# Kernel optimization log

Hardware: AMD Instinct MI355X
Metric: run time of the kernel (lower is better)

Reference implementation:

```python
import math
import jax, jax.numpy as jnp
import numpy as np

B, T, C = 2, 2048, 1024
N_HEAD = 16
HEAD_DIM = C // N_HEAD


def setup_inputs() -> dict:
    key = jax.random.key(0)
    k1, k2, k3 = jax.random.split(key, 3)
    std = 0.02
    return {
        "x": jax.random.normal(k1, (B, T, C), dtype=jnp.float32),
        "W_qkv": jax.random.normal(k2, (3 * C, C), dtype=jnp.float32) * std,
        "b_qkv": jnp.zeros((3 * C,), dtype=jnp.float32),
        "W_proj": jax.random.normal(k3, (C, C), dtype=jnp.float32) * std,
        "b_proj": jnp.zeros((C,), dtype=jnp.float32),
    }


def reference(x, W_qkv, b_qkv, W_proj, b_proj):
    Bs, Ts, Cs = x.shape
    # qkv projection, split as [3][n_head][head_dim] along last dim (matches torch view order)
    qkv = (x @ W_qkv.T + b_qkv).reshape(Bs, Ts, 3, N_HEAD, HEAD_DIM)
    qkv = qkv.transpose(0, 3, 2, 1, 4)  # (B, H, 3, T, hd)
    q, k, v = qkv[:, :, 0], qkv[:, :, 1], qkv[:, :, 2]  # each (B, H, T, hd)
    scale = 1.0 / math.sqrt(HEAD_DIM)
    att = jnp.einsum('bhtd,bhsd->bhts', q, k) * scale  # (B, H, T, T)
    causal = jnp.tril(jnp.ones((Ts, Ts), dtype=bool))
    att = jnp.where(causal, att, -jnp.inf)
    att = jax.nn.softmax(att, axis=-1)
    y = jnp.einsum('bhts,bhsd->bhtd', att, v)  # (B, H, T, hd)
    y = y.transpose(0, 2, 1, 3).reshape(Bs, Ts, Cs)
    return y @ W_proj.T + b_proj
```

## Files before the change

### kernel.cpp

```cpp
#include <hip/hip_runtime.h>
#include <cstdint>

#define BDIM  2
#define TSEQ  2048
#define CDIM  1024
#define NHEAD 16
#define HDIM  64
#define C3    3072

typedef __attribute__((ext_vector_type(8))) short short8_t;
typedef __attribute__((ext_vector_type(4))) short short4_t;
typedef __attribute__((ext_vector_type(4))) float f32x4;

static __device__ __forceinline__ unsigned short f2bf(float f) {
  union { float f; unsigned u; } v; v.f = f;
  unsigned r = v.u + 0x7FFFu + ((v.u >> 16) & 1u);
  return (unsigned short)(r >> 16);
}
static __device__ __forceinline__ unsigned cvtpk_bf16(float lo, float hi) {
  unsigned r;
  asm("v_cvt_pk_bf16_f32 %0, %1, %2" : "=v"(r) : "v"(lo), "v"(hi));
  return r;
}
static __device__ __forceinline__ void g2lds16(const unsigned short* g,
                                               unsigned short* l) {
  __builtin_amdgcn_global_load_lds(
      (const __attribute__((address_space(1))) void*)g,
      (__attribute__((address_space(3))) void*)l, 16, 0, 0);
}

__device__ __forceinline__ int kk_idx(int row, int chunk) {
  return row * 64 + (((chunk ^ (row & 7)) & 7) << 3);
}
__device__ __forceinline__ int vv_idx(int d, int chunk) {
  return d * 64 + (((chunk ^ (d & 7) ^ ((d >> 3) & 7)) & 7) << 3);
}

__global__ __launch_bounds__(256) void f32_to_bf16_3(
    const float* __restrict__ x, const float* __restrict__ wq,
    const float* __restrict__ wp, unsigned short* __restrict__ outb,
    int n1, int n2, int n3)
{
  const int i = blockIdx.x * 256 + threadIdx.x;
  const float* src; unsigned short* dst; int j;
  if (i < n1)            { src = x;  dst = outb;                        j = i; }
  else if (i < n1 + n2)  { src = wq; dst = outb + (size_t)n1 * 4;       j = i - n1; }
  else if (i < n1+n2+n3) { src = wp; dst = outb + (size_t)(n1+n2) * 4;  j = i - n1 - n2; }
  else return;
  const float4 v = ((const float4*)src)[j];
  const unsigned lo = (unsigned)f2bf(v.x) | ((unsigned)f2bf(v.y) << 16);
  const unsigned hi = (unsigned)f2bf(v.z) | ((unsigned)f2bf(v.w) << 16);
  ((uint2*)dst)[j] = make_uint2(lo, hi);
}

template <int FJ, bool OUT_BF16, int MWPE>
__global__ __launch_bounds__(256, MWPE) void gemm_bt_mfma(
    const unsigned short* __restrict__ A, const unsigned short* __restrict__ B,
    const float* __restrict__ bias, void* __restrict__ Cv,
    int M, int N, int K)
{
  __shared__ unsigned short As[128 * 64];
  __shared__ unsigned short Bs[FJ * 32 * 64];

  const int tid  = threadIdx.x;
  const int lane = tid & 63;
  const int wv   = tid >> 6;
  const int wr   = wv >> 1, wc = wv & 1;
  const int l15  = lane & 15, g = lane >> 4;
  const int bn = blockIdx.x, bm = blockIdx.y;

  const int srow = tid >> 3;
  const int chg  = (tid & 7) ^ (srow & 7);
  const unsigned short* Ab = A + (size_t)(bm * 128 + srow) * K + chg * 8;
  const unsigned short* Bb = B + (size_t)(bn * (FJ * 32) + srow) * K + chg * 8;

  f32x4 acc[4][FJ];
#pragma unroll
  for (int i = 0; i < 4; ++i)
#pragma unroll
    for (int j = 0; j < FJ; ++j) acc[i][j] = (f32x4){0.f, 0.f, 0.f, 0.f};

  for (int k0 = 0; k0 < K; k0 += 64) {
    __syncthreads();
#pragma unroll
    for (int c = 0; c < 4; ++c)
      g2lds16(Ab + (size_t)(c * 32) * K + k0, &As[c * 2048 + wv * 512]);
#pragma unroll
    for (int c = 0; c < FJ; ++c)
      g2lds16(Bb + (size_t)(c * 32) * K + k0, &Bs[c * 2048 + wv * 512]);
    __syncthreads();

#pragma unroll
    for (int kk = 0; kk < 2; ++kk) {
      short8_t af[4], bf[FJ];
#pragma unroll
      for (int i = 0; i < 4; ++i)
        af[i] = *(const short8_t*)&As[kk_idx(wr * 64 + i * 16 + l15, kk * 4 + g)];
#pragma unroll
      for (int j = 0; j < FJ; ++j)
        bf[j] = *(const short8_t*)&Bs[kk_idx(wc * (FJ * 16) + j * 16 + l15, kk * 4 + g)];
#pragma unroll
      for (int i = 0; i < 4; ++i)
#pragma unroll
        for (int j = 0; j < FJ; ++j)
          acc[i][j] = __builtin_amdgcn_mfma_f32_16x16x32_bf16(af[i], bf[j], acc[i][j], 0, 0, 0);
    }
  }

#pragma unroll
  for (int j = 0; j < FJ; ++j) {
    const int col = bn * (FJ * 32) + wc * (FJ * 16) + j * 16 + l15;
    const float bj = bias[col];
#pragma unroll
    for (int i = 0; i < 4; ++i) {
#pragma unroll
      for (int r = 0; r < 4; ++r) {
        const int row = bm * 128 + wr * 64 + i * 16 + g * 4 + r;
        const float v = acc[i][j][r] + bj;
        if (OUT_BF16) ((unsigned short*)Cv)[(size_t)row * N + col] = f2bf(v);
        else          ((float*)Cv)[(size_t)row * N + col] = v;
      }
    }
  }
}

__global__ __launch_bounds__(512, 8) void attn_mfma(
    const unsigned short* __restrict__ qkv, unsigned short* __restrict__ yb)
{
  __shared__ unsigned short SM[21504];
  unsigned short* Ks = SM;
  unsigned short* Vt = SM + 8192;
  unsigned short* Ps = SM + 16384;

  const int tid  = threadIdx.x;
  const int lane = tid & 63;
  const int wv   = tid >> 6;
  const int qs   = wv & 3;
  const int kvh  = wv >> 2;
  const int l15  = lane & 15, g = lane >> 4;

  const int nfl = blockIdx.x;
  const int x   = (nfl >> 3) & 15;
  const int grp = (nfl & 7) | ((nfl >> 7) << 3);
  const int h = grp & 15, b = grp >> 4;

  const unsigned short* kbase = qkv + (size_t)(b * TSEQ) * C3 + CDIM + h * HDIM;
  const unsigned short* vbase = kbase + CDIM;
  unsigned short* Pw = &Ps[wv * 640];

  const float SC2 = 0.18033688011112042f;
  const float THR = 11.5415603f;

  const int skv = tid >> 3, sc = tid & 7;
  const int kwo = kk_idx(skv, sc);
  const int vs = tid >> 4, dh = (tid >> 3) & 1, va = tid & 7;
  int vwo[4];
#pragma unroll
  for (int j = 0; j < 4; ++j)
    vwo[j] = vv_idx(va * 8 + dh * 4 + j, vs >> 2) + ((2 * vs) & 7);

  int tg = 0;

  for (int ph = 0; ph < 2; ++ph) {
    const int qt   = ph ? (31 - x) : x;
    const int wq0  = qt * 64 + qs * 16;
    const int q_hi = wq0 + 15;
    const int qg   = wq0 + l15;

    short8_t qf[2];
#pragma unroll
    for (int kk = 0; kk < 2; ++kk)
      qf[kk] = *(const short8_t*)(qkv +
          (size_t)(b * TSEQ + wq0 + l15) * C3 + h * HDIM + kk * 32 + g * 8);

    f32x4 O[4];
#pragma unroll
    for (int n = 0; n < 4; ++n) O[n] = (f32x4){0.f, 0.f, 0.f, 0.f};
    float Mr = 0.0f, Lr = 0.f;

    const unsigned short* kptr  = kbase + (size_t)skv * C3 + sc * 8;
    const unsigned short* vptr0 = vbase + (size_t)(2 * vs) * C3 + va * 8 + dh * 4;
    const unsigned short* vptr1 = vptr0 + C3;
    short8_t pk  = *(const short8_t*)(kptr);
    short4_t pv0 = *(const short4_t*)(vptr0);
    short4_t pv1 = *(const short4_t*)(vptr1);

    for (int t = 0; t < qt; ++t) {
      const int par = tg & 1;
      unsigned short* Kc = &Ks[par * 4096];
      unsigned short* Vc = &Vt[par * 4096];
      tg++;
      *(short8_t*)&Kc[kwo] = pk;
      {
        const unsigned short* e0 = (const unsigned short*)&pv0;
        const unsigned short* e1 = (const unsigned short*)&pv1;
#pragma unroll
        for (int j = 0; j < 4; ++j)
          *(unsigned*)&Vc[vwo[j]] = (unsigned)e0[j] | ((unsigned)e1[j] << 16);
      }
      __syncthreads();
      kptr  += (size_t)64 * C3;
      vptr0 += (size_t)64 * C3;
      vptr1 += (size_t)64 * C3;
      pk  = *(const short8_t*)(kptr);
      pv0 = *(const short4_t*)(vptr0);
      pv1 = *(const short4_t*)(vptr1);

      f32x4 s[2];
#pragma unroll
      for (int n = 0; n < 2; ++n) s[n] = (f32x4){0.f, 0.f, 0.f, 0.f};
      __builtin_amdgcn_s_setprio(1);
#pragma unroll
      for (int n = 0; n < 2; ++n) {
#pragma unroll
        for (int kk = 0; kk < 2; ++kk) {
          const short8_t kf =
              *(const short8_t*)&Kc[kk_idx(kvh * 32 + n * 16 + l15, kk * 4 + g)];
          s[n] = __builtin_amdgcn_mfma_f32_16x16x32_bf16(kf, qf[kk], s[n], 0, 0, 0);
        }
      }
      __builtin_amdgcn_s_setprio(0);

      float mt = -3.0e38f, rs = 0.f;
#pragma unroll
      for (int n = 0; n < 2; ++n)
#pragma unroll
        for (int r = 0; r < 4; ++r) mt = fmaxf(mt, s[n][r]);
#pragma unroll
      for (int n = 0; n < 2; ++n)
#pragma unroll
        for (int r = 0; r < 4; ++r) {
          const float p = __builtin_amdgcn_exp2f(fmaf(s[n][r], SC2, -Mr));
          s[n][r] = p;
          rs += p;
        }
#pragma unroll
      for (int n = 0; n < 2; ++n) {
        const unsigned u0 = cvtpk_bf16(s[n][0], s[n][1]);
        const unsigned u1 = cvtpk_bf16(s[n][2], s[n][3]);
        *(uint2*)&Pw[l15 * 40 + n * 16 + (g << 2)] = make_uint2(u0, u1);
      }
      mt *= SC2;
      mt = fmaxf(mt, __shfl_xor(mt, 16));
      mt = fmaxf(mt, __shfl_xor(mt, 32));
      if (__any(mt > Mr + THR)) {
        const float nm = fmaxf(Mr, mt);
        const float al = __builtin_amdgcn_exp2f(Mr - nm);
        Lr *= al;
        rs *= al;
        float alq[4];
#pragma unroll
        for (int r = 0; r < 4; ++r) alq[r] = __shfl(al, (g << 2) + r);
#pragma unroll
        for (int n = 0; n < 4; ++n)
#pragma unroll
          for (int r = 0; r < 4; ++r) O[n][r] *= alq[r];
        Mr = nm;
#pragma unroll
        for (int n = 0; n < 2; ++n) {
#pragma unroll
          for (int r = 0; r < 4; ++r) s[n][r] *= al;
          const unsigned u0 = cvtpk_bf16(s[n][0], s[n][1]);
          const unsigned u1 = cvtpk_bf16(s[n][2], s[n][3]);
          *(uint2*)&Pw[l15 * 40 + n * 16 + (g << 2)] = make_uint2(u0, u1);
        }
      }

      const short8_t pf = *(const short8_t*)&Pw[l15 * 40 + g * 8];
      __builtin_amdgcn_s_setprio(1);
#pragma unroll
      for (int n = 0; n < 4; ++n) {
        const short8_t vf = *(const short8_t*)&Vc[vv_idx(n * 16 + l15, kvh * 4 + g)];
        O[n] = __builtin_amdgcn_mfma_f32_16x16x32_bf16(pf, vf, O[n], 0, 0, 0);
      }
      __builtin_amdgcn_s_setprio(0);

      rs += __shfl_xor(rs, 16);
      rs += __shfl_xor(rs, 32);
      Lr += rs;
    }

    {
      const int t = qt;
      const int par = tg & 1;
      unsigned short* Kc = &Ks[par * 4096];
      unsigned short* Vc = &Vt[par * 4096];
      tg++;
      *(short8_t*)&Kc[kwo] = pk;
      {
        const unsigned short* e0 = (const unsigned short*)&pv0;
        const unsigned short* e1 = (const unsigned short*)&pv1;
#pragma unroll
        for (int j = 0; j < 4; ++j)
          *(unsigned*)&Vc[vwo[j]] = (unsigned)e0[j] | ((unsigned)e1[j] << 16);
      }
      __syncthreads();
      const int kvw0 = t * 64 + kvh * 32;
      if (kvw0 <= q_hi) {
        const int nl = (q_hi - kvw0) >> 4;
        const int nlim = (nl > 1) ? 1 : nl;

        f32x4 s[2];
#pragma unroll
        for (int n = 0; n < 2; ++n) s[n] = (f32x4){0.f, 0.f, 0.f, 0.f};
        __builtin_amdgcn_s_setprio(1);
#pragma unroll
        for (int n = 0; n < 2; ++n) {
          if (n <= nlim) {
#pragma unroll
            for (int kk = 0; kk < 2; ++kk) {
              const short8_t kf =
                  *(const short8_t*)&Kc[kk_idx(kvh * 32 + n * 16 + l15, kk * 4 + g)];
              s[n] = __builtin_amdgcn_mfma_f32_16x16x32_bf16(kf, qf[kk], s[n], 0, 0, 0);
            }
          }
        }
        __builtin_amdgcn_s_setprio(0);

        float mt = -3.0e38f;
#pragma unroll
        for (int n = 0; n < 2; ++n) {
          if (n <= nlim) {
            const int kvb = kvw0 + n * 16 + g * 4;
            const bool needmask = (kvw0 + n * 16 + 15 > wq0);
#pragma unroll
            for (int r = 0; r < 4; ++r) {
              float v = s[n][r] * SC2;
              if (needmask && (kvb + r > qg)) v = -3.0e38f;
              s[n][r] = v;
              mt = fmaxf(mt, v);
            }
          }
        }
        float rs = 0.f;
#pragma unroll
        for (int n = 0; n < 2; ++n) {
          if (n <= nlim) {
#pragma unroll
            for (int r = 0; r < 4; ++r) {
              const float p = __builtin_amdgcn_exp2f(s[n][r] - Mr);
              s[n][r] = p;
              rs += p;
            }
          }
        }
#pragma unroll
        for (int n = 0; n < 2; ++n) {
          const unsigned u0 = cvtpk_bf16(s[n][0], s[n][1]);
          const unsigned u1 = cvtpk_bf16(s[n][2], s[n][3]);
          *(uint2*)&Pw[l15 * 40 + n * 16 + (g << 2)] = make_uint2(u0, u1);
        }
        mt = fmaxf(mt, __shfl_xor(mt, 16));
        mt = fmaxf(mt, __shfl_xor(mt, 32));
        if (__any(mt > Mr + THR)) {
          const float nm = fmaxf(Mr, mt);
          const float al = __builtin_amdgcn_exp2f(Mr - nm);
          Lr *= al;
          rs *= al;
          float alq[4];
#pragma unroll
          for (int r = 0; r < 4; ++r) alq[r] = __shfl(al, (g << 2) + r);
#pragma unroll
          for (int n = 0; n < 4; ++n)
#pragma unroll
            for (int r = 0; r < 4; ++r) O[n][r] *= alq[r];
          Mr = nm;
#pragma unroll
          for (int n = 0; n < 2; ++n) {
            if (n <= nlim) {
#pragma unroll
              for (int r = 0; r < 4; ++r) s[n][r] *= al;
            }
            const unsigned u0 = cvtpk_bf16(s[n][0], s[n][1]);
            const unsigned u1 = cvtpk_bf16(s[n][2], s[n][3]);
            *(uint2*)&Pw[l15 * 40 + n * 16 + (g << 2)] = make_uint2(u0, u1);
          }
        }

        const short8_t pf = *(const short8_t*)&Pw[l15 * 40 + g * 8];
        __builtin_amdgcn_s_setprio(1);
#pragma unroll
        for (int n = 0; n < 4; ++n) {
          const short8_t vf = *(const short8_t*)&Vc[vv_idx(n * 16 + l15, kvh * 4 + g)];
          O[n] = __builtin_amdgcn_mfma_f32_16x16x32_bf16(pf, vf, O[n], 0, 0, 0);
        }
        __builtin_amdgcn_s_setprio(0);

        rs += __shfl_xor(rs, 16);
        rs += __shfl_xor(rs, 32);
        Lr += rs;
      }
    }

    __syncthreads();
    {
      float* Cb = (float*)SM;
      const int slot = (qs * 64 + lane) * 18;
      if (kvh == 1) {
#pragma unroll
        for (int n = 0; n < 4; ++n)
#pragma unroll
          for (int r = 0; r < 4; ++r) Cb[slot + n * 4 + r] = O[n][r];
        Cb[slot + 16] = Mr;
        Cb[slot + 17] = Lr;
      }
    }
    __syncthreads();
    if (kvh == 0) {
      const float* Cb = (const float*)SM;
      const int slot = (qs * 64 + lane) * 18;
      const float m2 = Cb[slot + 16], l2 = Cb[slot + 17];
      const float m  = fmaxf(Mr, m2);
      const float a1 = __builtin_amdgcn_exp2f(Mr - m);
      const float a2 = __builtin_amdgcn_exp2f(m2 - m);
      const float inv = 1.0f / (Lr * a1 + l2 * a2);
      const float fa = a1 * inv, fb = a2 * inv;
      float faq[4], fbq[4];
#pragma unroll
      for (int r = 0; r < 4; ++r) {
        faq[r] = __shfl(fa, (g << 2) + r);
        fbq[r] = __shfl(fb, (g << 2) + r);
      }
#pragma unroll
      for (int n = 0; n < 4; ++n)
#pragma unroll
        for (int r = 0; r < 4; ++r) {
          const float o2 = Cb[slot + n * 4 + r];
          const size_t row = (size_t)(b * TSEQ + wq0 + (g << 2) + r);
          yb[row * CDIM + h * HDIM + n * 16 + l15] =
              f2bf(O[n][r] * faq[r] + o2 * fbq[r]);
        }
    }
    __syncthreads();
  }
}

extern "C" void kernel_launch(void* const* d_in, const int* in_sizes, int n_in,
                              void* d_out, int out_size, void* d_ws, size_t ws_size,
                              hipStream_t stream)
{
  const float* x     = (const float*)d_in[0];
  const float* Wqkv  = (const float*)d_in[1];
  const float* bqkv  = (const float*)d_in[2];
  const float* Wproj = (const float*)d_in[3];
  const float* bproj = (const float*)d_in[4];
  float* out = (float*)d_out;

  const int M = BDIM * TSEQ;
  unsigned short* qkv = (unsigned short*)d_ws;
  unsigned short* yb  = qkv + (size_t)M * C3;
  unsigned short* xb  = yb  + (size_t)M * CDIM;
  unsigned short* wqb = xb  + (size_t)M * CDIM;
  unsigned short* wpb = wqb + (size_t)C3 * CDIM;

  const int n1 = M * CDIM / 4, n2 = C3 * CDIM / 4, n3 = CDIM * CDIM / 4;
  f32_to_bf16_3<<<(n1 + n2 + n3 + 255) / 256, 256, 0, stream>>>(
      x, Wqkv, Wproj, xb, n1, n2, n3);

  gemm_bt_mfma<4, true, 3><<<dim3(C3 / 128, M / 128), 256, 0, stream>>>(
      xb, wqb, bqkv, (void*)qkv, M, C3, CDIM);

  attn_mfma<<<dim3(512, 1, 1), 512, 0, stream>>>(qkv, yb);

  gemm_bt_mfma<2, false, 2><<<dim3(CDIM / 64, M / 128), 256, 0, stream>>>(
      yb, wpb, bproj, (void*)out, M, CDIM, CDIM);
}
```

Baseline: 97.27 us.

## Process two KV tiles per barrier with quad-buffered K/V shared memory

The attention loop now stages two 64-row K/V tiles per iteration into four LDS buffers. This halves the number of __syncthreads barriers and doubles the global prefetch depth. In exchange LDS use grows from about 42KB to about 74KB per block, which may limit occupancy. The final diagonal step now handles a 128-row chunk and may load tiles past the causal boundary.

Result: no change. 96.95 us (-0.3%).

```diff
diff --git a/kernel.cpp b/kernel.cpp
--- a/kernel.cpp
+++ b/kernel.cpp
@@ -127,10 +127,10 @@
 __global__ __launch_bounds__(512, 8) void attn_mfma(
     const unsigned short* __restrict__ qkv, unsigned short* __restrict__ yb)
 {
-  __shared__ unsigned short SM[21504];
+  __shared__ unsigned short SM[37888];
   unsigned short* Ks = SM;
-  unsigned short* Vt = SM + 8192;
-  unsigned short* Ps = SM + 16384;
+  unsigned short* Vt = SM + 16384;
+  unsigned short* Ps = SM + 32768;
 
   const int tid  = threadIdx.x;
   const int lane = tid & 63;
@@ -159,13 +159,12 @@
   for (int j = 0; j < 4; ++j)
     vwo[j] = vv_idx(va * 8 + dh * 4 + j, vs >> 2) + ((2 * vs) & 7);
 
-  int tg = 0;
-
   for (int ph = 0; ph < 2; ++ph) {
     const int qt   = ph ? (31 - x) : x;
     const int wq0  = qt * 64 + qs * 16;
     const int q_hi = wq0 + 15;
     const int qg   = wq0 + l15;
+    const int fastc = qt >> 1;
 
     short8_t qf[2];
 #pragma unroll
@@ -180,123 +179,149 @@
 
     const unsigned short* kptr  = kbase + (size_t)skv * C3 + sc * 8;
     const unsigned short* vptr0 = vbase + (size_t)(2 * vs) * C3 + va * 8 + dh * 4;
-    const unsigned short* vptr1 = vptr0 + C3;
-    short8_t pk  = *(const short8_t*)(kptr);
+    short8_t pk0 = *(const short8_t*)(kptr);
+    short8_t pk1 = *(const short8_t*)(kptr + (size_t)64 * C3);
     short4_t pv0 = *(const short4_t*)(vptr0);
-    short4_t pv1 = *(const short4_t*)(vptr1);
-
-    for (int t = 0; t < qt; ++t) {
-      const int par = tg & 1;
-      unsigned short* Kc = &Ks[par * 4096];
-      unsigned short* Vc = &Vt[par * 4096];
-      tg++;
-      *(short8_t*)&Kc[kwo] = pk;
+    short4_t pv1 = *(const short4_t*)(vptr0 + C3);
+    short4_t pv2 = *(const short4_t*)(vptr0 + (size_t)64 * C3);
+    short4_t pv3 = *(const short4_t*)(vptr0 + (size_t)65 * C3);
+
+    for (int c = 0; c < fastc; ++c) {
+      const int p2 = (c & 1) << 1;
       {
+        unsigned short* K0 = &Ks[p2 * 4096];
+        unsigned short* K1 = &Ks[(p2 + 1) * 4096];
+        unsigned short* V0 = &Vt[p2 * 4096];
+        unsigned short* V1 = &Vt[(p2 + 1) * 4096];
+        *(short8_t*)&K0[kwo] = pk0;
+        *(short8_t*)&K1[kwo] = pk1;
         const unsigned short* e0 = (const unsigned short*)&pv0;
         const unsigned short* e1 = (const unsigned short*)&pv1;
-#pragma unroll
-        for (int j = 0; j < 4; ++j)
-          *(unsigned*)&Vc[vwo[j]] = (unsigned)e0[j] | ((unsigned)e1[j] << 16);
+        const unsigned short* e2 = (const unsigned short*)&pv2;
+        const unsigned short* e3 = (const unsigned short*)&pv3;
+#pragma unroll
+        for (int j = 0; j < 4; ++j) {
+          *(unsigned*)&V0[vwo[j]] = (unsigned)e0[j] | ((unsigned)e1[j] << 16);
+          *(unsigned*)&V1[vwo[j]] = (unsigned)e2[j] | ((unsigned)e3[j] << 16);
+        }
       }
       __syncthreads();
-      kptr  += (size_t)64 * C3;
-      vptr0 += (size_t)64 * C3;
-      vptr1 += (size_t)64 * C3;
-      pk  = *(const short8_t*)(kptr);
+      kptr  += (size_t)128 * C3;
+      vptr0 += (size_t)128 * C3;
+      pk0 = *(const short8_t*)(kptr);
+      pk1 = *(const short8_t*)(kptr + (size_t)64 * C3);
       pv0 = *(const short4_t*)(vptr0);
-      pv1 = *(const short4_t*)(vptr1);
-
-      f32x4 s[2];
-#pragma unroll
-      for (int n = 0; n < 2; ++n) s[n] = (f32x4){0.f, 0.f, 0.f, 0.f};
-      __builtin_amdgcn_s_setprio(1);
-#pragma unroll
-      for (int n = 0; n < 2; ++n) {
-#pragma unroll
-        for (int kk = 0; kk < 2; ++kk) {
-          const short8_t kf =
-              *(const short8_t*)&Kc[kk_idx(kvh * 32 + n * 16 + l15, kk * 4 + g)];
-          s[n] = __builtin_amdgcn_mfma_f32_16x16x32_bf16(kf, qf[kk], s[n], 0, 0, 0);
-        }
-      }
-      __builtin_amdgcn_s_setprio(0);
-
-      float mt = -3.0e38f, rs = 0.f;
-#pragma unroll
-      for (int n = 0; n < 2; ++n)
-#pragma unroll
-        for (int r = 0; r < 4; ++r) mt = fmaxf(mt, s[n][r]);
-#pragma unroll
-      for (int n = 0; n < 2; ++n)
-#pragma unroll
-        for (int r = 0; r < 4; ++r) {
-          const float p = __builtin_amdgcn_exp2f(fmaf(s[n][r], SC2, -Mr));
-          s[n][r] = p;
-          rs += p;
-        }
-#pragma unroll
-      for (int n = 0; n < 2; ++n) {
-        const unsigned u0 = cvtpk_bf16(s[n][0], s[n][1]);
-        const unsigned u1 = cvtpk_bf16(s[n][2], s[n][3]);
-        *(uint2*)&Pw[l15 * 40 + n * 16 + (g << 2)] = make_uint2(u0, u1);
-      }
-      mt *= SC2;
-      mt = fmaxf(mt, __shfl_xor(mt, 16));
-      mt = fmaxf(mt, __shfl_xor(mt, 32));
-      if (__any(mt > Mr + THR)) {
-        const float nm = fmaxf(Mr, mt);
-        const float al = __builtin_amdgcn_exp2f(Mr - nm);
-        Lr *= al;
-        rs *= al;
-        float alq[4];
-#pragma unroll
-        for (int r = 0; r < 4; ++r) alq[r] = __shfl(al, (g << 2) + r);
-#pragma unroll
-        for (int n = 0; n < 4; ++n)
-#pragma unroll
-          for (int r = 0; r < 4; ++r) O[n][r] *= alq[r];
-        Mr = nm;
-#pragma unroll
-        for (int n = 0; n < 2; ++n) {
-#pragma unroll
-          for (int r = 0; r < 4; ++r) s[n][r] *= al;
+      pv1 = *(const short4_t*)(vptr0 + C3);
+      pv2 = *(const short4_t*)(vptr0 + (size_t)64 * C3);
+      pv3 = *(const short4_t*)(vptr0 + (size_t)65 * C3);
+
+#pragma unroll
+      for (int sub = 0; sub < 2; ++sub) {
+        const unsigned short* Kc = &Ks[(p2 + sub) * 4096];
+        const unsigned short* Vc = &Vt[(p2 + sub) * 4096];
+
+        f32x4 s[2];
+#pragma unroll
+        for (int n = 0; n < 2; ++n) s[n] = (f32x4){0.f, 0.f, 0.f, 0.f};
+        __builtin_amdgcn_s_setprio(1);
+#pragma unroll
+        for (int n = 0; n < 2; ++n) {
+#pragma unroll
+          for (int kk = 0; kk < 2; ++kk) {
+            const short8_t kf =
+                *(const short8_t*)&Kc[kk_idx(kvh * 32 + n * 16 + l15, kk * 4 + g)];
+            s[n] = __builtin_amdgcn_mfma_f32_16x16x32_bf16(kf, qf[kk], s[n], 0, 0, 0);
+          }
+        }
+        __builtin_amdgcn_s_setprio(0);
+
+        float mt = -3.0e38f, rs = 0.f;
+#pragma unroll
+        for (int n = 0; n < 2; ++n)
+#pragma unroll
+          for (int r = 0; r < 4; ++r) mt = fmaxf(mt, s[n][r]);
+#pragma unroll
+        for (int n = 0; n < 2; ++n)
+#pragma unroll
+          for (int r = 0; r < 4; ++r) {
+            const float p = __builtin_amdgcn_exp2f(fmaf(s[n][r], SC2, -Mr));
+            s[n][r] = p;
+            rs += p;
+          }
+#pragma unroll
+        for (int n = 0; n < 2; ++n) {
           const unsigned u0 = cvtpk_bf16(s[n][0], s[n][1]);
           const unsigned u1 = cvtpk_bf16(s[n][2], s[n][3]);
           *(uint2*)&Pw[l15 * 40 + n * 16 + (g << 2)] = make_uint2(u0, u1);
         }
-      }
-
-      const short8_t pf = *(const short8_t*)&Pw[l15 * 40 + g * 8];
-      __builtin_amdgcn_s_setprio(1);
-#pragma unroll
-      for (int n = 0; n < 4; ++n) {
-        const short8_t vf = *(const short8_t*)&Vc[vv_idx(n * 16 + l15, kvh * 4 + g)];
-        O[n] = __builtin_amdgcn_mfma_f32_16x16x32_bf16(pf, vf, O[n], 0, 0, 0);
-      }
-      __builtin_amdgcn_s_setprio(0);
-
-      rs += __shfl_xor(rs, 16);
-      rs += __shfl_xor(rs, 32);
-      Lr += rs;
+        mt *= SC2;
+        mt = fmaxf(mt, __shfl_xor(mt, 16));
+        mt = fmaxf(mt, __shfl_xor(mt, 32));
+        if (__any(mt > Mr + THR)) {
+          const float nm = fmaxf(Mr, mt);
+          const float al = __builtin_amdgcn_exp2f(Mr - nm);
+          Lr *= al;
+          rs *= al;
+          float alq[4];
+#pragma unroll
+          for (int r = 0; r < 4; ++r) alq[r] = __shfl(al, (g << 2) + r);
+#pragma unroll
+          for (int n = 0; n < 4; ++n)
+#pragma unroll
+            for (int r = 0; r < 4; ++r) O[n][r] *= alq[r];
+          Mr = nm;
+#pragma unroll
+          for (int n = 0; n < 2; ++n) {
+#pragma unroll
+            for (int r = 0; r < 4; ++r) s[n][r] *= al;
+            const unsigned u0 = cvtpk_bf16(s[n][0], s[n][1]);
+            const unsigned u1 = cvtpk_bf16(s[n][2], s[n][3]);
+            *(uint2*)&Pw[l15 * 40 + n * 16 + (g << 2)] = make_uint2(u0, u1);
+          }
+        }
+
+        const short8_t pf = *(const short8_t*)&Pw[l15 * 40 + g * 8];
+        __builtin_amdgcn_s_setprio(1);
+#pragma unroll
+        for (int n = 0; n < 4; ++n) {
+          const short8_t vf = *(const short8_t*)&Vc[vv_idx(n * 16 + l15, kvh * 4 + g)];
+          O[n] = __builtin_amdgcn_mfma_f32_16x16x32_bf16(pf, vf, O[n], 0, 0, 0);
+        }
+        __builtin_amdgcn_s_setprio(0);
+
+        rs += __shfl_xor(rs, 16);
+        rs += __shfl_xor(rs, 32);
+        Lr += rs;
+      }
     }
 
     {
-      const int t = qt;
-      const int par = tg & 1;
-      unsigned short* Kc = &Ks[par * 4096];
-      unsigned short* Vc = &Vt[par * 4096];
-      tg++;
-      *(short8_t*)&Kc[kwo] = pk;
+      const int p2 = (fastc & 1) << 1;
       {
+        unsigned short* K0 = &Ks[p2 * 4096];
+        unsigned short* K1 = &Ks[(p2 + 1) * 4096];
+        unsigned short* V0 = &Vt[p2 * 4096];
+        unsigned short* V1 = &Vt[(p2 + 1) * 4096];
+        *(short8_t*)&K0[kwo] = pk0;
+        *(short8_t*)&K1[kwo] = pk1;
         const unsigned short* e0 = (const unsigned short*)&pv0;
         const unsigned short* e1 = (const unsigned short*)&pv1;
-#pragma unroll
-        for (int j = 0; j < 4; ++j)
-          *(unsigned*)&Vc[vwo[j]] = (unsigned)e0[j] | ((unsigned)e1[j] << 16);
+        const unsigned short* e2 = (const unsigned short*)&pv2;
+        const unsigned short* e3 = (const unsigned short*)&pv3;
+#pragma unroll
+        for (int j = 0; j < 4; ++j) {
+          *(unsigned*)&V0[vwo[j]] = (unsigned)e0[j] | ((unsigned)e1[j] << 16);
+          *(unsigned*)&V1[vwo[j]] = (unsigned)e2[j] | ((unsigned)e3[j] << 16);
+        }
       }
       __syncthreads();
-      const int kvw0 = t * 64 + kvh * 32;
-      if (kvw0 <= q_hi) {
+
+#pragma unroll
+      for (int sub = 0; sub < 2; ++sub) {
+        const int kvw0 = fastc * 128 + sub * 64 + kvh * 32;
+        if (kvw0 > q_hi) continue;
+        const unsigned short* Kc = &Ks[(p2 + sub) * 4096];
+        const unsigned short* Vc = &Vt[(p2 + sub) * 4096];
         const int nl = (q_hi - kvw0) >> 4;
         const int nlim = (nl > 1) ? 1 : nl;
 
```

## Halve attention block to 4 waves, each wave handling 32 query rows

Applied to the files above, without the earlier changes.

The attention kernel now launches 256 threads per block instead of 512, and each wave processes two 16-row query tiles. This lets every K/V fragment read from LDS feed two MFMAs, and each thread loads twice as much K/V from global per tile. It aims to cut LDS read traffic and sync overhead per unit of work. The cost is more registers per thread (doubled O and S accumulators), fewer waves per CU to hide latency, and a lower occupancy hint in the launch bounds.

New measurement: 99.23 us. 1.02x slower.

```diff
diff --git a/kernel.cpp b/kernel.cpp
--- a/kernel.cpp
+++ b/kernel.cpp
@@ -124,7 +124,7 @@
   }
 }
 
-__global__ __launch_bounds__(512, 8) void attn_mfma(
+__global__ __launch_bounds__(256, 2) void attn_mfma(
     const unsigned short* __restrict__ qkv, unsigned short* __restrict__ yb)
 {
   __shared__ unsigned short SM[21504];
@@ -135,8 +135,8 @@
   const int tid  = threadIdx.x;
   const int lane = tid & 63;
   const int wv   = tid >> 6;
-  const int qs   = wv & 3;
-  const int kvh  = wv >> 2;
+  const int qs   = wv & 1;
+  const int kvh  = wv >> 1;
   const int l15  = lane & 15, g = lane >> 4;
 
   const int nfl = blockIdx.x;
@@ -146,69 +146,76 @@
 
   const unsigned short* kbase = qkv + (size_t)(b * TSEQ) * C3 + CDIM + h * HDIM;
   const unsigned short* vbase = kbase + CDIM;
-  unsigned short* Pw = &Ps[wv * 640];
+  unsigned short* Pw = &Ps[wv * 1280];
 
   const float SC2 = 0.18033688011112042f;
   const float THR = 11.5415603f;
 
-  const int skv = tid >> 3, sc = tid & 7;
-  const int kwo = kk_idx(skv, sc);
-  const int vs = tid >> 4, dh = (tid >> 3) & 1, va = tid & 7;
-  int vwo[4];
-#pragma unroll
-  for (int j = 0; j < 4; ++j)
-    vwo[j] = vv_idx(va * 8 + dh * 4 + j, vs >> 2) + ((2 * vs) & 7);
+  const int skv = tid >> 2;
+  const int sa  = (tid & 3) * 2;
+  const int kw0 = kk_idx(skv, sa + 0);
+  const int kw1 = kk_idx(skv, sa + 1);
+  const int vs = tid >> 3, va = tid & 7;
+  int vwo[8];
+#pragma unroll
+  for (int j = 0; j < 8; ++j)
+    vwo[j] = vv_idx(va * 8 + j, vs >> 2) + ((2 * vs) & 7);
 
   int tg = 0;
 
   for (int ph = 0; ph < 2; ++ph) {
     const int qt   = ph ? (31 - x) : x;
-    const int wq0  = qt * 64 + qs * 16;
-    const int q_hi = wq0 + 15;
-    const int qg   = wq0 + l15;
-
-    short8_t qf[2];
-#pragma unroll
-    for (int kk = 0; kk < 2; ++kk)
-      qf[kk] = *(const short8_t*)(qkv +
-          (size_t)(b * TSEQ + wq0 + l15) * C3 + h * HDIM + kk * 32 + g * 8);
-
-    f32x4 O[4];
-#pragma unroll
-    for (int n = 0; n < 4; ++n) O[n] = (f32x4){0.f, 0.f, 0.f, 0.f};
-    float Mr = 0.0f, Lr = 0.f;
-
-    const unsigned short* kptr  = kbase + (size_t)skv * C3 + sc * 8;
-    const unsigned short* vptr0 = vbase + (size_t)(2 * vs) * C3 + va * 8 + dh * 4;
+    const int wq0  = qt * 64 + qs * 32;
+
+    short8_t qf[2][2];
+#pragma unroll
+    for (int qm = 0; qm < 2; ++qm)
+#pragma unroll
+      for (int kk = 0; kk < 2; ++kk)
+        qf[qm][kk] = *(const short8_t*)(qkv +
+            (size_t)(b * TSEQ + wq0 + qm * 16 + l15) * C3 + h * HDIM + kk * 32 + g * 8);
+
+    f32x4 O[2][4];
+#pragma unroll
+    for (int qm = 0; qm < 2; ++qm)
+#pragma unroll
+      for (int n = 0; n < 4; ++n) O[qm][n] = (f32x4){0.f, 0.f, 0.f, 0.f};
+    float Mr[2] = {0.0f, 0.0f}, Lr[2] = {0.f, 0.f};
+
+    const unsigned short* kptr  = kbase + (size_t)skv * C3 + sa * 8;
+    const unsigned short* vptr0 = vbase + (size_t)(2 * vs) * C3 + va * 8;
     const unsigned short* vptr1 = vptr0 + C3;
-    short8_t pk  = *(const short8_t*)(kptr);
-    short4_t pv0 = *(const short4_t*)(vptr0);
-    short4_t pv1 = *(const short4_t*)(vptr1);
+    short8_t pk0 = *(const short8_t*)(kptr);
+    short8_t pk1 = *(const short8_t*)(kptr + 8);
+    short8_t pv0 = *(const short8_t*)(vptr0);
+    short8_t pv1 = *(const short8_t*)(vptr1);
 
     for (int t = 0; t < qt; ++t) {
       const int par = tg & 1;
       unsigned short* Kc = &Ks[par * 4096];
       unsigned short* Vc = &Vt[par * 4096];
       tg++;
-      *(short8_t*)&Kc[kwo] = pk;
+      *(short8_t*)&Kc[kw0] = pk0;
+      *(short8_t*)&Kc[kw1] = pk1;
       {
         const unsigned short* e0 = (const unsigned short*)&pv0;
         const unsigned short* e1 = (const unsigned short*)&pv1;
 #pragma unroll
-        for (int j = 0; j < 4; ++j)
+        for (int j = 0; j < 8; ++j)
           *(unsigned*)&Vc[vwo[j]] = (unsigned)e0[j] | ((unsigned)e1[j] << 16);
       }
       __syncthreads();
       kptr  += (size_t)64 * C3;
       vptr0 += (size_t)64 * C3;
       vptr1 += (size_t)64 * C3;
-      pk  = *(const short8_t*)(kptr);
-      pv0 = *(const short4_t*)(vptr0);
-      pv1 = *(const short4_t*)(vptr1);
-
-      f32x4 s[2];
-#pragma unroll
-      for (int n = 0; n < 2; ++n) s[n] = (f32x4){0.f, 0.f, 0.f, 0.f};
+      pk0 = *(const short8_t*)(kptr); pk1 = *(const short8_t*)(kptr + 8);
+      pv0 = *(const short8_t*)(vptr0); pv1 = *(const short8_t*)(vptr1);
+
+      f32x4 s[2][2];
+#pragma unroll
+      for (int n = 0; n < 2; ++n)
+#pragma unroll
+        for (int qm = 0; qm < 2; ++qm) s[n][qm] = (f32x4){0.f, 0.f, 0.f, 0.f};
       __builtin_amdgcn_s_setprio(1);
 #pragma unroll
       for (int n = 0; n < 2; ++n) {
@@ -216,87 +223,107 @@
         for (int kk = 0; kk < 2; ++kk) {
           const short8_t kf =
               *(const short8_t*)&Kc[kk_idx(kvh * 32 + n * 16 + l15, kk * 4 + g)];
-          s[n] = __builtin_amdgcn_mfma_f32_16x16x32_bf16(kf, qf[kk], s[n], 0, 0, 0);
+#pragma unroll
+          for (int qm = 0; qm < 2; ++qm)
+            s[n][qm] = __builtin_amdgcn_mfma_f32_16x16x32_bf16(kf, qf[qm][kk], s[n][qm], 0, 0, 0);
         }
       }
       __builtin_amdgcn_s_setprio(0);
 
-      float mt = -3.0e38f, rs = 0.f;
-#pragma unroll
-      for (int n = 0; n < 2; ++n)
-#pragma unroll
-        for (int r = 0; r < 4; ++r) mt = fmaxf(mt, s[n][r]);
-#pragma unroll
-      for (int n = 0; n < 2; ++n)
-#pragma unroll
-        for (int r = 0; r < 4; ++r) {
-          const float p = __builtin_amdgcn_exp2f(fmaf(s[n][r], SC2, -Mr));
-          s[n][r] = p;
-          rs += p;
-        }
-#pragma unroll
-      for (int n = 0; n < 2; ++n) {
-        const unsigned u0 = cvtpk_bf16(s[n][0], s[n][1]);
-        const unsigned u1 = cvtpk_bf16(s[n][2], s[n][3]);
-        *(uint2*)&Pw[l15 * 40 + n * 16 + (g << 2)] = make_uint2(u0, u1);
-      }
-      mt *= SC2;
-      mt = fmaxf(mt, __shfl_xor(mt, 16));
-      mt = fmaxf(mt, __shfl_xor(mt, 32));
-      if (__any(mt > Mr + THR)) {
-        const float nm = fmaxf(Mr, mt);
-        const float al = __builtin_amdgcn_exp2f(Mr - nm);
-        Lr *= al;
-        rs *= al;
-        float alq[4];
-#pragma unroll
-        for (int r = 0; r < 4; ++r) alq[r] = __shfl(al, (g << 2) + r);
-#pragma unroll
-        for (int n = 0; n < 4; ++n)
-#pragma unroll
-          for (int r = 0; r < 4; ++r) O[n][r] *= alq[r];
-        Mr = nm;
+      float mt[2] = {-3.0e38f, -3.0e38f}, rs[2] = {0.f, 0.f};
+#pragma unroll
+      for (int qm = 0; qm < 2; ++qm) {
+#pragma unroll
+        for (int n = 0; n < 2; ++n)
+#pragma unroll
+          for (int r = 0; r < 4; ++r) mt[qm] = fmaxf(mt[qm], s[n][qm][r]);
+#pragma unroll
+        for (int n = 0; n < 2; ++n)
+#pragma unroll
+          for (int r = 0; r < 4; ++r) {
+            const float p = __builtin_amdgcn_exp2f(fmaf(s[n][qm][r], SC2, -Mr[qm]));
+            s[n][qm][r] = p;
+            rs[qm] += p;
+          }
 #pragma unroll
         for (int n = 0; n < 2; ++n) {
-#pragma unroll
-          for (int r = 0; r < 4; ++r) s[n][r] *= al;
-          const unsigned u0 = cvtpk_bf16(s[n][0], s[n][1]);
-          const unsigned u1 = cvtpk_bf16(s[n][2], s[n][3]);
-          *(uint2*)&Pw[l15 * 40 + n * 16 + (g << 2)] = make_uint2(u0, u1);
-        }
-      }
-
-      const short8_t pf = *(const short8_t*)&Pw[l15 * 40 + g * 8];
+          const unsigned u0 = cvtpk_bf16(s[n][qm][0], s[n][qm][1]);
+          const unsigned u1 = cvtpk_bf16(s[n][qm][2], s[n][qm][3]);
+          *(uint2*)&Pw[(qm * 16 + l15) * 40 + n * 16 + (g << 2)] = make_uint2(u0, u1);
+        }
+        mt[qm] *= SC2;
+      }
+      if (__any((mt[0] > Mr[0] + THR) || (mt[1] > Mr[1] + THR))) {
+#pragma unroll
+        for (int qm = 0; qm < 2; ++qm) {
+          float mq = mt[qm];
+          mq = fmaxf(mq, __shfl_xor(mq, 16));
+          mq = fmaxf(mq, __shfl_xor(mq, 32));
+          const float nm = fmaxf(Mr[qm], mq);
+          const float al = __builtin_amdgcn_exp2f(Mr[qm] - nm);
+          Lr[qm] *= al;
+          rs[qm] *= al;
+          float alq[4];
+#pragma unroll
+          for (int r = 0; r < 4; ++r) alq[r] = __shfl(al, (g << 2) + r);
+#pragma unroll
+          for (int n = 0; n < 4; ++n)
+#pragma unroll
+            for (int r = 0; r < 4; ++r) O[qm][n][r] *= alq[r];
+          Mr[qm] = nm;
+#pragma unroll
+          for (int n = 0; n < 2; ++n) {
+#pragma unroll
+            for (int r = 0; r < 4; ++r) s[n][qm][r] *= al;
+            const unsigned u0 = cvtpk_bf16(s[n][qm][0], s[n][qm][1]);
+            const unsigned u1 = cvtpk_bf16(s[n][qm][2], s[n][qm][3]);
+            *(uint2*)&Pw[(qm * 16 + l15) * 40 + n * 16 + (g << 2)] = make_uint2(u0, u1);
+          }
+        }
+      }
+
+      const short8_t pf0 = *(const short8_t*)&Pw[(0 * 16 + l15) * 40 + g * 8];
+      const short8_t pf1 = *(const short8_t*)&Pw[(1 * 16 + l15) * 40 + g * 8];
       __builtin_amdgcn_s_setprio(1);
 #pragma unroll
       for (int n = 0; n < 4; ++n) {
         const short8_t vf = *(const short8_t*)&Vc[vv_idx(n * 16 + l15, kvh * 4 + g)];
-        O[n] = __builtin_amdgcn_mfma_f32_16x16x32_bf16(pf, vf, O[n], 0, 0, 0);
+        O[0][n] = __builtin_amdgcn_mfma_f32_16x16x32_bf16(pf0, vf, O[0][n], 0, 0, 0);
+        O[1][n] = __builtin_amdgcn_mfma_f32_16x16x32_bf16(pf1, vf, O[1][n], 0, 0, 0);
       }
       __builtin_amdgcn_s_setprio(0);
 
-      rs += __shfl_xor(rs, 16);
-      rs += __shfl_xor(rs, 32);
-      Lr += rs;
+#pragma unroll
+      for (int qm = 0; qm < 2; ++qm) {
+        rs[qm] += __shfl_xor(rs[qm], 16);
+        rs[qm] += __shfl_xor(rs[qm], 32);
+        Lr[qm] += rs[qm];
+      }
     }
 
     {
-      const int t = qt;
       const int par = tg & 1;
       unsigned short* Kc = &Ks[par * 4096];
       unsigned short* Vc = &Vt[par * 4096];
       tg++;
-      *(short8_t*)&Kc[kwo] = pk;
+      *(short8_t*)&Kc[kw0] = pk0;
+      *(short8_t*)&Kc[kw1] = pk1;
       {
         const unsigned short* e0 = (const unsigned short*)&pv0;
         const unsigned short* e1 = (const unsigned short*)&pv1;
 #pragma unroll
-        for (int j = 0; j < 4; ++j)
+        for (int j = 0; j < 8; ++j)
           *(unsigned*)&Vc[vwo[j]] = (unsigned)e0[j] | ((unsigned)e1[j] << 16);
       }
       __syncthreads();
-      const int kvw0 = t * 64 + kvh * 32;
-      if (kvw0 <= q_hi) {
+      const int kvw0 = qt * 64 + kvh * 32;
+
+#pragma unroll
+      for (int qm = 0; qm < 2; ++qm) {
+        const int wq0m = wq0 + qm * 16;
+        const int q_hi = wq0m + 15;
+        const int qg   = wq0m + l15;
+        if (kvw0 > q_hi) continue;
         const int nl = (q_hi - kvw0) >> 4;
         const int nlim = (nl > 1) ? 1 : nl;
 
@@ -311,7 +338,7 @@
             for (int kk = 0; kk < 2; ++kk) {
               const short8_t kf =
                   *(const short8_t*)&Kc[kk_idx(kvh * 32 + n * 16 + l15, kk * 4 + g)];
-              s[n] = __builtin_amdgcn_mfma_f32_16x16x32_bf16(kf, qf[kk], s[n], 0, 0, 0);
+              s[n] = __builtin_amdgcn_mfma_f32_16x16x32_bf16(kf, qf[qm][kk], s[n], 0, 0, 0);
             }
           }
         }
@@ -322,7 +349,7 @@
         for (int n = 0; n < 2; ++n) {
           if (n <= nlim) {
             const int kvb = kvw0 + n * 16 + g * 4;
-            const bool needmask = (kvw0 + n * 16 + 15 > wq0);
+            const bool needmask = (kvw0 + n * 16 + 15 > wq0m);
 #pragma unroll
             for (int r = 0; r < 4; ++r) {
               float v = s[n][r] * SC2;
@@ -338,7 +365,7 @@
           if (n <= nlim) {
 #pragma unroll
             for (int r = 0; r < 4; ++r) {
-              const float p = __builtin_amdgcn_exp2f(s[n][r] - Mr);
+              const float p = __builtin_amdgcn_exp2f(s[n][r] - Mr[qm]);
               s[n][r] = p;
               rs += p;
             }
@@ -348,14 +375,14 @@
         for (int n = 0; n < 2; ++n) {
           const unsigned u0 = cvtpk_bf16(s[n][0], s[n][1]);
           const unsigned u1 = cvtpk_bf16(s[n][2], s[n][3]);
-          *(uint2*)&Pw[l15 * 40 + n * 16 + (g << 2)] = make_uint2(u0, u1);
+          *(uint2*)&Pw[(qm * 16 + l15) * 40 + n * 16 + (g << 2)] = make_uint2(u0, u1);
         }
         mt = fmaxf(mt, __shfl_xor(mt, 16));
         mt = fmaxf(mt, __shfl_xor(mt, 32));
-        if (__any(mt > Mr + THR)) {
-          const float nm = fmaxf(Mr, mt);
-          const float al = __builtin_amdgcn_exp2f(Mr - nm);
-          Lr *= al;
+        if (__any(mt > Mr[qm] + THR)) {
+          const float nm = fmaxf(Mr[qm], mt);
+          const float al = __builtin_amdgcn_exp2f(Mr[qm] - nm);
+          Lr[qm] *= al;
           rs *= al;
           float alq[4];
 #pragma unroll
@@ -363,8 +390,8 @@
 #pragma unroll
           for (int n = 0; n < 4; ++n)
 #pragma unroll
-            for (int r = 0; r < 4; ++r) O[n][r] *= alq[r];
-          Mr = nm;
+            for (int r = 0; r < 4; ++r) O[qm][n][r] *= alq[r];
+          Mr[qm] = nm;
 #pragma unroll
           for (int n = 0; n < 2; ++n) {
             if (n <= nlim) {
@@ -373,63 +400,69 @@
             }
             const unsigned u0 = cvtpk_bf16(s[n][0], s[n][1]);
             const unsigned u1 = cvtpk_bf16(s[n][2], s[n][3]);
-            *(uint2*)&Pw[l15 * 40 + n * 16 + (g << 2)] = make_uint2(u0, u1);
-          }
-        }
-
-        const short8_t pf = *(const short8_t*)&Pw[l15 * 40 + g * 8];
+            *(uint2*)&Pw[(qm * 16 + l15) * 40 + n * 16 + (g << 2)] = make_uint2(u0, u1);
+          }
+        }
+
+        const short8_t pf = *(const short8_t*)&Pw[(qm * 16 + l15) * 40 + g * 8];
         __builtin_amdgcn_s_setprio(1);
 #pragma unroll
         for (int n = 0; n < 4; ++n) {
           const short8_t vf = *(const short8_t*)&Vc[vv_idx(n * 16 + l15, kvh * 4 + g)];
-          O[n] = __builtin_amdgcn_mfma_f32_16x16x32_bf16(pf, vf, O[n], 0, 0, 0);
+          O[qm][n] = __builtin_amdgcn_mfma_f32_16x16x32_bf16(pf, vf, O[qm][n], 0, 0, 0);
         }
         __builtin_amdgcn_s_setprio(0);
 
         rs += __shfl_xor(rs, 16);
         rs += __shfl_xor(rs, 32);
-        Lr += rs;
+        Lr[qm] += rs;
       }
     }
 
     __syncthreads();
     {
       float* Cb = (float*)SM;
-      const int slot = (qs * 64 + lane) * 18;
       if (kvh == 1) {
 #pragma unroll
-        for (int n = 0; n < 4; ++n)
-#pragma unroll
-          for (int r = 0; r < 4; ++r) Cb[slot + n * 4 + r] = O[n][r];
-        Cb[slot + 16] = Mr;
-        Cb[slot + 17] = Lr;
+        for (int qm = 0; qm < 2; ++qm) {
+          const int slot = ((qs * 2 + qm) * 64 + lane) * 18;
+#pragma unroll
+          for (int n = 0; n < 4; ++n)
+#pragma unroll
+            for (int r = 0; r < 4; ++r) Cb[slot + n * 4 + r] = O[qm][n][r];
+          Cb[slot + 16] = Mr[qm];
+          Cb[slot + 17] = Lr[qm];
+        }
       }
     }
     __syncthreads();
     if (kvh == 0) {
       const float* Cb = (const float*)SM;
-      const int slot = (qs * 64 + lane) * 18;
-      const float m2 = Cb[slot + 16], l2 = Cb[slot + 17];
-      const float m  = fmaxf(Mr, m2);
-      const float a1 = __builtin_amdgcn_exp2f(Mr - m);
-      const float a2 = __builtin_amdgcn_exp2f(m2 - m);
-      const float inv = 1.0f / (Lr * a1 + l2 * a2);
-      const float fa = a1 * inv, fb = a2 * inv;
-      float faq[4], fbq[4];
-#pragma unroll
-      for (int r = 0; r < 4; ++r) {
-        faq[r] = __shfl(fa, (g << 2) + r);
-        fbq[r] = __shfl(fb, (g << 2) + r);
-      }
-#pragma unroll
-      for (int n = 0; n < 4; ++n)
+#pragma unroll
+      for (int qm = 0; qm < 2; ++qm) {
+        const int slot = ((qs * 2 + qm) * 64 + lane) * 18;
+        const float m2 = Cb[slot + 16], l2 = Cb[slot + 17];
+        const float m  = fmaxf(Mr[qm], m2);
+        const float a1 = __builtin_amdgcn_exp2f(Mr[qm] - m);
+        const float a2 = __builtin_amdgcn_exp2f(m2 - m);
+        const float inv = 1.0f / (Lr[qm] * a1 + l2 * a2);
+        const float fa = a1 * inv, fb = a2 * inv;
+        float faq[4], fbq[4];
 #pragma unroll
         for (int r = 0; r < 4; ++r) {
-          const float o2 = Cb[slot + n * 4 + r];
-          const size_t row = (size_t)(b * TSEQ + wq0 + (g << 2) + r);
-          yb[row * CDIM + h * HDIM + n * 16 + l15] =
-              f2bf(O[n][r] * faq[r] + o2 * fbq[r]);
-        }
+          faq[r] = __shfl(fa, (g << 2) + r);
+          fbq[r] = __shfl(fb, (g << 2) + r);
+        }
+#pragma unroll
+        for (int n = 0; n < 4; ++n)
+#pragma unroll
+          for (int r = 0; r < 4; ++r) {
+            const float o2 = Cb[slot + n * 4 + r];
+            const size_t row = (size_t)(b * TSEQ + wq0 + qm * 16 + (g << 2) + r);
+            yb[row * CDIM + h * HDIM + n * 16 + l15] =
+                f2bf(O[qm][n][r] * faq[r] + o2 * fbq[r]);
+          }
+      }
     }
     __syncthreads();
   }
@@ -460,7 +493,7 @@
   gemm_bt_mfma<4, true, 3><<<dim3(C3 / 128, M / 128), 256, 0, stream>>>(
       xb, wqb, bqkv, (void*)qkv, M, C3, CDIM);
 
-  attn_mfma<<<dim3(512, 1, 1), 512, 0, stream>>>(qkv, yb);
+  attn_mfma<<<dim3(512, 1, 1), 256, 0, stream>>>(qkv, yb);
 
   gemm_bt_mfma<2, false, 2><<<dim3(CDIM / 64, M / 128), 256, 0, stream>>>(
       yb, wpb, bproj, (void*)out, M, CDIM, CDIM);
```
